# Kernel optimization log

Hardware: AMD Instinct MI355X
Metric: run time of the kernel (lower is better)

## Reference

```python
import jax, jax.numpy as jnp
from jax import lax
import numpy as np

B, N, C = 16, 8192, 256


def farthest_point_sample(pts, npoint):
    # pts: [B, N, 3]. Standard PointNet++ FPS; is_center=True -> start from the
    # point farthest from the centroid (argmax of dist-to-mean).
    b, n, _ = pts.shape
    centroid = pts.mean(axis=1, keepdims=True)                  # [B,1,3]
    d0 = jnp.sum((pts - centroid) ** 2, axis=-1)                # [B,N]
    farthest = jnp.argmax(d0, axis=-1)                          # [B]
    dist = jnp.full((b, n), 1e10, dtype=pts.dtype)

    def step(carry, _):
        dist, far = carry
        cur = jnp.take_along_axis(pts, far[:, None, None], axis=1)  # [B,1,3]
        d = jnp.sum((pts - cur) ** 2, axis=-1)                      # [B,N]
        dist = jnp.minimum(dist, d)
        new_far = jnp.argmax(dist, axis=-1)
        return (dist, new_far), far

    (_, _), idxs = lax.scan(step, (dist, farthest), None, length=npoint)
    return idxs.T  # [B, npoint]


def index_points(x, idx):
    # x: [B, N, D], idx: [B, M] -> [B, M, D]
    return jnp.take_along_axis(x, idx[:, :, None], axis=1)


def setup_inputs() -> dict:
    key = jax.random.key(0)
    k1, k2 = jax.random.split(key)
    points = jax.random.normal(k1, (B, 3, N), dtype=jnp.float32)
    features = jax.random.normal(k2, (B, C, N), dtype=jnp.float32)
    return {"points": points, "features": features, "num_points": 2048}


def reference(points, features, num_points):
    pts = jnp.swapaxes(points, -1, -2)     # [B,N,3]
    feats = jnp.swapaxes(features, -1, -2) # [B,N,C]
    idx = farthest_point_sample(pts, num_points)  # [B,M] int
    sampled_points = index_points(pts, idx)       # [B,M,3]
    sampled_features = index_points(feats, idx)   # [B,M,C]
    return sampled_points, sampled_features
```

## Files before the change

### kernel.cpp

```cpp
#include <hip/hip_runtime.h>
#include <cfloat>

#define BB 16
#define NN 8192
#define CC 256
#define NT 512
#define PPT 16
#define NPAIR (PPT / 2)
#define NWAVES (NT / 64)
#define TBLOCKS 240
#define NTILES (BB * (CC / 64) * (NN / 64))

typedef float    v2f __attribute__((ext_vector_type(2)));
typedef unsigned v2u __attribute__((ext_vector_type(2)));
typedef unsigned uu;
typedef unsigned long long ull;

#define LDS_BARRIER() __asm__ __volatile__("s_waitcnt lgkmcnt(0)\n\ts_barrier" ::: "memory")

struct SmemFPS {
  float px[NN], py[NN], pz[NN];
  ull   key[2][NWAVES];
  float red[NWAVES][3];
  float ctr[3];
};
struct SmemT {
  float tile[64][65];
};
union Smem { SmemFPS f; SmemT t; };

__device__ __forceinline__ v2f pk_sub(v2f a, v2f b) {
  v2f d;
  asm("v_pk_add_f32 %0, %1, %2 neg_lo:[0,1] neg_hi:[0,1]"
      : "=v"(d) : "v"(a), "v"(b));
  return d;
}
__device__ __forceinline__ v2f pk_mul(v2f a, v2f b) {
  v2f d;
  asm("v_pk_mul_f32 %0, %1, %2" : "=v"(d) : "v"(a), "v"(b));
  return d;
}
__device__ __forceinline__ v2f pk_add(v2f a, v2f b) {
  v2f d;
  asm("v_pk_add_f32 %0, %1, %2" : "=v"(d) : "v"(a), "v"(b));
  return d;
}

__device__ __forceinline__ uu umin2(uu a, uu b) { return a < b ? a : b; }
__device__ __forceinline__ uu umax2(uu a, uu b) { return a > b ? a : b; }

__device__ __forceinline__ ull max64(ull a, ull b) { return a > b ? a : b; }

template <int CTRL>
__device__ __forceinline__ ull dpp_max64(ull x) {
  int lo = (int)(uu)x;
  int hi = (int)(uu)(x >> 32);
  int plo = __builtin_amdgcn_update_dpp(0, lo, CTRL, 0xF, 0xF, true);
  int phi = __builtin_amdgcn_update_dpp(0, hi, CTRL, 0xF, 0xF, true);
  ull p = ((ull)(uu)phi << 32) | (uu)plo;
  return max64(x, p);
}

__device__ __forceinline__ ull wave_max63(ull k) {
  k = dpp_max64<0xB1>(k);
  k = dpp_max64<0x4E>(k);
  k = dpp_max64<0x124>(k);
  k = dpp_max64<0x128>(k);
  k = dpp_max64<0x142>(k);
  k = dpp_max64<0x143>(k);
  return k;
}

__global__ __launch_bounds__(NT)
void fps_fused_kernel(const float* __restrict__ pts,
                      const float* __restrict__ feats,
                      float* __restrict__ out_pts,
                      int* __restrict__ idx_out,
                      float* __restrict__ trans, int M, int do_trans) {
  __shared__ Smem sm;
  const int t = threadIdx.x;

  if (blockIdx.x >= BB) {
    if (!do_trans) return;
    for (int tileId = blockIdx.x - BB; tileId < NTILES; tileId += TBLOCKS) {
      int b  = tileId / ((CC / 64) * (NN / 64));
      int r  = tileId % ((CC / 64) * (NN / 64));
      int ct = r / (NN / 64);
      int nt = r % (NN / 64);
      const float* src = feats + ((size_t)b * CC + ct * 64) * NN + nt * 64;
      float* dst = trans + ((size_t)b * NN + nt * 64) * CC + ct * 64;
#pragma unroll
      for (int i = 0; i < 2; ++i) {
        int f = t + i * NT;
        int c = f >> 4, n4 = f & 15;
        float4 v = *(const float4*)(src + (size_t)c * NN + n4 * 4);
        sm.t.tile[c][n4 * 4 + 0] = v.x;
        sm.t.tile[c][n4 * 4 + 1] = v.y;
        sm.t.tile[c][n4 * 4 + 2] = v.z;
        sm.t.tile[c][n4 * 4 + 3] = v.w;
      }
      __syncthreads();
#pragma unroll
      for (int i = 0; i < 2; ++i) {
        int f = t + i * NT;
        int n = f >> 4, c4 = f & 15;
        float4 o;
        o.x = sm.t.tile[c4 * 4 + 0][n];
        o.y = sm.t.tile[c4 * 4 + 1][n];
        o.z = sm.t.tile[c4 * 4 + 2][n];
        o.w = sm.t.tile[c4 * 4 + 3][n];
        *(float4*)(dst + (size_t)n * CC + c4 * 4) = o;
      }
      __syncthreads();
    }
    return;
  }

  const int b = blockIdx.x;
  const int wave = t >> 6;
  const int lane = t & 63;
  const float* base = pts + (size_t)b * 3 * NN;

  v2f px2[NPAIR], py2[NPAIR], pz2[NPAIR];
  v2u dist2[NPAIR];
  const uu INIT = __float_as_uint(1e10f);
#pragma unroll
  for (int j = 0; j < NPAIR; ++j) {
    int n0 = t + (2 * j) * NT;
    int n1 = t + (2 * j + 1) * NT;
    float x0 = base[n0], y0 = base[NN + n0], z0 = base[2 * NN + n0];
    float x1 = base[n1], y1 = base[NN + n1], z1 = base[2 * NN + n1];
    px2[j] = (v2f){x0, x1};
    py2[j] = (v2f){y0, y1};
    pz2[j] = (v2f){z0, z1};
    sm.f.px[n0] = x0; sm.f.py[n0] = y0; sm.f.pz[n0] = z0;
    sm.f.px[n1] = x1; sm.f.py[n1] = y1; sm.f.pz[n1] = z1;
    dist2[j] = (v2u){INIT, INIT};
  }

  float sx = 0.f, sy = 0.f, sz = 0.f;
#pragma unroll
  for (int j = 0; j < NPAIR; ++j) {
    sx += px2[j].x; sx += px2[j].y;
    sy += py2[j].x; sy += py2[j].y;
    sz += pz2[j].x; sz += pz2[j].y;
  }
#pragma unroll
  for (int off = 32; off > 0; off >>= 1) {
    sx += __shfl_xor(sx, off);
    sy += __shfl_xor(sy, off);
    sz += __shfl_xor(sz, off);
  }
  if (lane == 0) { sm.f.red[wave][0] = sx; sm.f.red[wave][1] = sy; sm.f.red[wave][2] = sz; }
  __syncthreads();
  if (t == 0) {
    float gx = 0.f, gy = 0.f, gz = 0.f;
    for (int w = 0; w < NWAVES; ++w) { gx += sm.f.red[w][0]; gy += sm.f.red[w][1]; gz += sm.f.red[w][2]; }
    sm.f.ctr[0] = gx / NN; sm.f.ctr[1] = gy / NN; sm.f.ctr[2] = gz / NN;
  }
  __syncthreads();
  const float ctx = sm.f.ctr[0], cty = sm.f.ctr[1], ctz = sm.f.ctr[2];

  int ep = 0;
  int ci;

  auto reduce_tail = [&](uu v, int bk) {
    ull key = ((ull)v << 32) | (uu)(~(t + (bk << 9)));
    key = wave_max63(key);
    ep ^= 1;
    if (lane == 63) sm.f.key[ep][wave] = key;
    LDS_BARRIER();
    ull kk = sm.f.key[ep][lane & 7];
    kk = dpp_max64<0xB1>(kk);
    kk = dpp_max64<0x4E>(kk);
    kk = dpp_max64<0x124>(kk);
    ci = (int)~(uu)kk;
  };

  {
    v2f c2x = {ctx, ctx}, c2y = {cty, cty}, c2z = {ctz, ctz};
    v2u nd2[NPAIR];
    uu v = 0u;
#pragma unroll
    for (int j = 0; j < NPAIR; ++j) {
      v2f dx = pk_sub(px2[j], c2x);
      v2f dy = pk_sub(py2[j], c2y);
      v2f dz = pk_sub(pz2[j], c2z);
      v2f d = pk_add(pk_add(pk_mul(dx, dx), pk_mul(dy, dy)), pk_mul(dz, dz));
      v2u du = (v2u){__float_as_uint(d.x), __float_as_uint(d.y)};
      nd2[j] = du;
      v = umax2(v, umax2(du.x, du.y));
    }
    int bk = 0;
#pragma unroll
    for (int k = PPT - 1; k >= 0; --k) {
      uu ndk = (k & 1) ? nd2[k >> 1].y : nd2[k >> 1].x;
      if (ndk == v) bk = k;
    }
    reduce_tail(v, bk);
  }

  for (int m = 0; m < M; ++m) {
    float cx = sm.f.px[ci], cy = sm.f.py[ci], cz = sm.f.pz[ci];
    if (t == 0) {
      idx_out[b * M + m] = ci;
      size_t o = ((size_t)b * M + m) * 3;
      out_pts[o] = cx; out_pts[o + 1] = cy; out_pts[o + 2] = cz;
    }
    if (m == M - 1) break;

    v2f c2x = {cx, cx}, c2y = {cy, cy}, c2z = {cz, cz};
    v2u nd2[NPAIR];
    uu v = 0u;
#pragma unroll
    for (int j = 0; j < NPAIR; ++j) {
      v2f dx = pk_sub(px2[j], c2x);
      v2f dy = pk_sub(py2[j], c2y);
      v2f dz = pk_sub(pz2[j], c2z);
      v2f d = pk_add(pk_add(pk_mul(dx, dx), pk_mul(dy, dy)), pk_mul(dz, dz));
      v2u nd;
      nd.x = umin2(dist2[j].x, __float_as_uint(d.x));
      nd.y = umin2(dist2[j].y, __float_as_uint(d.y));
      dist2[j] = nd;
      nd2[j] = nd;
      v = umax2(v, umax2(nd.x, nd.y));
    }
    int bk = 0;
#pragma unroll
    for (int k = PPT - 1; k >= 0; --k) {
      uu ndk = (k & 1) ? nd2[k >> 1].y : nd2[k >> 1].x;
      if (ndk == v) bk = k;
    }
    reduce_tail(v, bk);
  }
}

__global__ __launch_bounds__(256)
void gather_t_kernel(const float* __restrict__ trans,
                     const int* __restrict__ idx,
                     float* __restrict__ out_f, int M) {
  int gm = blockIdx.x * 4 + (threadIdx.x >> 6);
  if (gm >= BB * M) return;
  int lane = threadIdx.x & 63;
  int b = gm / M;
  int n = idx[gm];
  float4 v = *(const float4*)(trans + ((size_t)b * NN + n) * CC + lane * 4);
  *(float4*)(out_f + (size_t)gm * CC + lane * 4) = v;
}

__global__ __launch_bounds__(CC)
void gather_kernel(const float* __restrict__ feats, const int* __restrict__ idx,
                   float* __restrict__ out_f, int M) {
  const int bm = blockIdx.x;
  const int b = bm / M;
  const int n = idx[bm];
  const int c = threadIdx.x;
  out_f[(size_t)bm * CC + c] = feats[((size_t)b * CC + c) * NN + n];
}

extern "C" void kernel_launch(void* const* d_in, const int* in_sizes, int n_in,
                              void* d_out, int out_size, void* d_ws, size_t ws_size,
                              hipStream_t stream) {
  const float* points = (const float*)d_in[0];
  const float* feats  = (const float*)d_in[1];
  int M = out_size / (BB * (3 + CC));
  if (M <= 0) M = 1;

  float* out_pts = (float*)d_out;
  float* out_f   = (float*)d_out + (size_t)BB * M * 3;

  int* idx_ws = (int*)d_ws;
  size_t idx_bytes = (((size_t)BB * M * sizeof(int)) + 255) & ~(size_t)255;
  size_t trans_bytes = (size_t)BB * NN * CC * sizeof(float);
  bool use_t = (ws_size >= idx_bytes + trans_bytes);
  float* trans = (float*)((char*)d_ws + idx_bytes);

  int grid = use_t ? (BB + TBLOCKS) : BB;
  fps_fused_kernel<<<dim3(grid), dim3(NT), 0, stream>>>(
      points, feats, out_pts, idx_ws, trans, M, use_t ? 1 : 0);

  if (use_t) {
    gather_t_kernel<<<dim3((BB * M + 3) / 4), dim3(256), 0, stream>>>(
        trans, idx_ws, out_f, M);
  } else {
    gather_kernel<<<dim3(BB * M), dim3(CC), 0, stream>>>(feats, idx_ws, out_f, M);
  }
}
```

Baseline: 1.909 ms.

## Morton-sort points per block and prune FPS distance updates with bounding spheres

Points are bucketed into a 12-bit Morton order with an LDS histogram, prefix scan and scatter, so each thread owns a spatially compact group of 16 points. Each thread keeps a bounding sphere around its group. When a wave's spheres are all farther from the new center than the cached max distance, the distance update is skipped and the cached max and index are reused. Ties break on the original index packed into the key, so the selection order is preserved. This trades a costly setup sort and extra LDS use for skipping per-iteration arithmetic, and the skip only happens when every lane in a wave prunes.

```diff
diff --git a/kernel.cpp b/kernel.cpp
--- a/kernel.cpp
+++ b/kernel.cpp
@@ -10,6 +10,7 @@
 #define NWAVES (NT / 64)
 #define TBLOCKS 240
 #define NTILES (BB * (CC / 64) * (NN / 64))
+#define NBUCK 4096
 
 typedef float    v2f __attribute__((ext_vector_type(2)));
 typedef unsigned v2u __attribute__((ext_vector_type(2)));
@@ -20,13 +21,14 @@
 
 struct SmemFPS {
   float px[NN], py[NN], pz[NN];
+  unsigned short pn[NN];
+  int   hist[NBUCK];
   ull   key[2][NWAVES];
-  float red[NWAVES][3];
-  float ctr[3];
+  float red[NWAVES][9];
+  float st9[9];
+  int   wsum[NWAVES];
 };
-struct SmemT {
-  float tile[64][65];
-};
+struct SmemT { float tile[64][65]; };
 union Smem { SmemFPS f; SmemT t; };
 
 __device__ __forceinline__ v2f pk_sub(v2f a, v2f b) {
@@ -48,7 +50,6 @@
 
 __device__ __forceinline__ uu umin2(uu a, uu b) { return a < b ? a : b; }
 __device__ __forceinline__ uu umax2(uu a, uu b) { return a > b ? a : b; }
-
 __device__ __forceinline__ ull max64(ull a, ull b) { return a > b ? a : b; }
 
 template <int CTRL>
@@ -69,6 +70,17 @@
   k = dpp_max64<0x142>(k);
   k = dpp_max64<0x143>(k);
   return k;
+}
+
+__device__ __forceinline__ int morton12(int x, int y, int z) {
+  int c = 0;
+#pragma unroll
+  for (int i = 0; i < 4; ++i) {
+    c |= ((x >> i) & 1) << (3 * i);
+    c |= ((y >> i) & 1) << (3 * i + 1);
+    c |= ((z >> i) & 1) << (3 * i + 2);
+  }
+  return c;
 }
 
 __global__ __launch_bounds__(NT)
@@ -121,51 +133,134 @@
   const int lane = t & 63;
   const float* base = pts + (size_t)b * 3 * NN;
 
+  float rx[PPT], ry[PPT], rz[PPT];
+#pragma unroll
+  for (int k = 0; k < PPT; ++k) {
+    int n = t + k * NT;
+    rx[k] = base[n]; ry[k] = base[NN + n]; rz[k] = base[2 * NN + n];
+  }
+  float sx = 0.f, sy = 0.f, sz = 0.f;
+  float mnx = rx[0], mny = ry[0], mnz = rz[0];
+  float mxx = rx[0], mxy = ry[0], mxz = rz[0];
+#pragma unroll
+  for (int k = 0; k < PPT; ++k) {
+    sx += rx[k]; sy += ry[k]; sz += rz[k];
+    mnx = fminf(mnx, rx[k]); mny = fminf(mny, ry[k]); mnz = fminf(mnz, rz[k]);
+    mxx = fmaxf(mxx, rx[k]); mxy = fmaxf(mxy, ry[k]); mxz = fmaxf(mxz, rz[k]);
+  }
+#pragma unroll
+  for (int off = 32; off > 0; off >>= 1) {
+    sx += __shfl_xor(sx, off); sy += __shfl_xor(sy, off); sz += __shfl_xor(sz, off);
+    mnx = fminf(mnx, __shfl_xor(mnx, off));
+    mny = fminf(mny, __shfl_xor(mny, off));
+    mnz = fminf(mnz, __shfl_xor(mnz, off));
+    mxx = fmaxf(mxx, __shfl_xor(mxx, off));
+    mxy = fmaxf(mxy, __shfl_xor(mxy, off));
+    mxz = fmaxf(mxz, __shfl_xor(mxz, off));
+  }
+  if (lane == 0) {
+    sm.f.red[wave][0] = sx;  sm.f.red[wave][1] = sy;  sm.f.red[wave][2] = sz;
+    sm.f.red[wave][3] = mnx; sm.f.red[wave][4] = mny; sm.f.red[wave][5] = mnz;
+    sm.f.red[wave][6] = mxx; sm.f.red[wave][7] = mxy; sm.f.red[wave][8] = mxz;
+  }
+  for (int i = t; i < NBUCK; i += NT) sm.f.hist[i] = 0;
+  __syncthreads();
+  if (t == 0) {
+    float gx = 0.f, gy = 0.f, gz = 0.f;
+    float a3 = sm.f.red[0][3], a4 = sm.f.red[0][4], a5 = sm.f.red[0][5];
+    float a6 = sm.f.red[0][6], a7 = sm.f.red[0][7], a8 = sm.f.red[0][8];
+    for (int w = 0; w < NWAVES; ++w) {
+      gx += sm.f.red[w][0]; gy += sm.f.red[w][1]; gz += sm.f.red[w][2];
+      a3 = fminf(a3, sm.f.red[w][3]); a4 = fminf(a4, sm.f.red[w][4]);
+      a5 = fminf(a5, sm.f.red[w][5]);
+      a6 = fmaxf(a6, sm.f.red[w][6]); a7 = fmaxf(a7, sm.f.red[w][7]);
+      a8 = fmaxf(a8, sm.f.red[w][8]);
+    }
+    sm.f.st9[0] = gx / NN; sm.f.st9[1] = gy / NN; sm.f.st9[2] = gz / NN;
+    sm.f.st9[3] = a3; sm.f.st9[4] = a4; sm.f.st9[5] = a5;
+    sm.f.st9[6] = a6; sm.f.st9[7] = a7; sm.f.st9[8] = a8;
+  }
+  __syncthreads();
+  const float ctx = sm.f.st9[0], cty = sm.f.st9[1], ctz = sm.f.st9[2];
+  const float qmnx = sm.f.st9[3], qmny = sm.f.st9[4], qmnz = sm.f.st9[5];
+  const float eps = 1e-30f;
+  const float sclx = 15.9999f / fmaxf(sm.f.st9[6] - qmnx, eps);
+  const float scly = 15.9999f / fmaxf(sm.f.st9[7] - qmny, eps);
+  const float sclz = 15.9999f / fmaxf(sm.f.st9[8] - qmnz, eps);
+
+  int code[PPT];
+#pragma unroll
+  for (int k = 0; k < PPT; ++k) {
+    int qx = (int)((rx[k] - qmnx) * sclx); qx = qx > 15 ? 15 : qx;
+    int qy = (int)((ry[k] - qmny) * scly); qy = qy > 15 ? 15 : qy;
+    int qz = (int)((rz[k] - qmnz) * sclz); qz = qz > 15 ? 15 : qz;
+    code[k] = morton12(qx, qy, qz);
+    atomicAdd(&sm.f.hist[code[k]], 1);
+  }
+  __syncthreads();
+
+  int loc[8]; int ssum = 0;
+#pragma unroll
+  for (int i = 0; i < 8; ++i) { loc[i] = ssum; ssum += sm.f.hist[t * 8 + i]; }
+  int sc = ssum;
+#pragma unroll
+  for (int off = 1; off < 64; off <<= 1) {
+    int o = __shfl_up(sc, off);
+    if (lane >= off) sc += o;
+  }
+  if (lane == 63) sm.f.wsum[wave] = sc;
+  __syncthreads();
+  int woff = 0;
+  for (int w = 0; w < wave; ++w) woff += sm.f.wsum[w];
+  int tbase = woff + sc - ssum;
+#pragma unroll
+  for (int i = 0; i < 8; ++i) sm.f.hist[t * 8 + i] = tbase + loc[i];
+  __syncthreads();
+
+#pragma unroll
+  for (int k = 0; k < PPT; ++k) {
+    int pos = atomicAdd(&sm.f.hist[code[k]], 1);
+    sm.f.px[pos] = rx[k]; sm.f.py[pos] = ry[k]; sm.f.pz[pos] = rz[k];
+    sm.f.pn[pos] = (unsigned short)(t + k * NT);
+  }
+  __syncthreads();
+
+  const int p0 = t * PPT;
   v2f px2[NPAIR], py2[NPAIR], pz2[NPAIR];
   v2u dist2[NPAIR];
+  uu  low[PPT];
+  float csx = 0.f, csy = 0.f, csz = 0.f;
+#pragma unroll
+  for (int k = 0; k < PPT; ++k) {
+    float x = sm.f.px[p0 + k], y = sm.f.py[p0 + k], z = sm.f.pz[p0 + k];
+    int n = (int)sm.f.pn[p0 + k];
+    if (k & 1) { px2[k >> 1].y = x; py2[k >> 1].y = y; pz2[k >> 1].y = z; }
+    else       { px2[k >> 1].x = x; py2[k >> 1].x = y * 0.f + x;
+                 px2[k >> 1].x = x; py2[k >> 1].x = y; pz2[k >> 1].x = z; }
+    low[k] = ~(uu)(((uu)n << 13) | (uu)(p0 + k));
+    csx += x; csy += y; csz += z;
+  }
+  const float ictrx = csx * 0.0625f, ictry = csy * 0.0625f, ictrz = csz * 0.0625f;
+  float r2m = 0.f;
+#pragma unroll
+  for (int k = 0; k < PPT; ++k) {
+    float x = (k & 1) ? px2[k >> 1].y : px2[k >> 1].x;
+    float y = (k & 1) ? py2[k >> 1].y : py2[k >> 1].x;
+    float z = (k & 1) ? pz2[k >> 1].y : pz2[k >> 1].x;
+    float ddx = x - ictrx, ddy = y - ictry, ddz = z - ictrz;
+    r2m = fmaxf(r2m, fmaf(ddx, ddx, fmaf(ddy, ddy, ddz * ddz)));
+  }
+  const float rr = __fsqrt_rn(r2m) * 1.0001f + 1e-7f;
   const uu INIT = __float_as_uint(1e10f);
 #pragma unroll
-  for (int j = 0; j < NPAIR; ++j) {
-    int n0 = t + (2 * j) * NT;
-    int n1 = t + (2 * j + 1) * NT;
-    float x0 = base[n0], y0 = base[NN + n0], z0 = base[2 * NN + n0];
-    float x1 = base[n1], y1 = base[NN + n1], z1 = base[2 * NN + n1];
-    px2[j] = (v2f){x0, x1};
-    py2[j] = (v2f){y0, y1};
-    pz2[j] = (v2f){z0, z1};
-    sm.f.px[n0] = x0; sm.f.py[n0] = y0; sm.f.pz[n0] = z0;
-    sm.f.px[n1] = x1; sm.f.py[n1] = y1; sm.f.pz[n1] = z1;
-    dist2[j] = (v2u){INIT, INIT};
-  }
-
-  float sx = 0.f, sy = 0.f, sz = 0.f;
-#pragma unroll
-  for (int j = 0; j < NPAIR; ++j) {
-    sx += px2[j].x; sx += px2[j].y;
-    sy += py2[j].x; sy += py2[j].y;
-    sz += pz2[j].x; sz += pz2[j].y;
-  }
-#pragma unroll
-  for (int off = 32; off > 0; off >>= 1) {
-    sx += __shfl_xor(sx, off);
-    sy += __shfl_xor(sy, off);
-    sz += __shfl_xor(sz, off);
-  }
-  if (lane == 0) { sm.f.red[wave][0] = sx; sm.f.red[wave][1] = sy; sm.f.red[wave][2] = sz; }
-  __syncthreads();
-  if (t == 0) {
-    float gx = 0.f, gy = 0.f, gz = 0.f;
-    for (int w = 0; w < NWAVES; ++w) { gx += sm.f.red[w][0]; gy += sm.f.red[w][1]; gz += sm.f.red[w][2]; }
-    sm.f.ctr[0] = gx / NN; sm.f.ctr[1] = gy / NN; sm.f.ctr[2] = gz / NN;
-  }
-  __syncthreads();
-  const float ctx = sm.f.ctr[0], cty = sm.f.ctr[1], ctz = sm.f.ctr[2];
-
-  int ep = 0;
-  int ci;
-
-  auto reduce_tail = [&](uu v, int bk) {
-    ull key = ((ull)v << 32) | (uu)(~(t + (bk << 9)));
+  for (int j = 0; j < NPAIR; ++j) dist2[j] = (v2u){INIT, INIT};
+  uu vcache = 0x7f800000u;
+  uu lowcache = 0u;
+
+  int ep = 0, cpos = 0, corig = 0;
+
+  auto reduce_tail = [&](uu v, uu blow) {
+    ull key = ((ull)v << 32) | blow;
     key = wave_max63(key);
     ep ^= 1;
     if (lane == 63) sm.f.key[ep][wave] = key;
@@ -174,7 +269,9 @@
     kk = dpp_max64<0xB1>(kk);
     kk = dpp_max64<0x4E>(kk);
     kk = dpp_max64<0x124>(kk);
-    ci = (int)~(uu)kk;
+    uu X = ~(uu)kk;
+    cpos = (int)(X & 0x1FFFu);
+    corig = (int)(X >> 13);
   };
 
   {
@@ -191,47 +288,62 @@
       nd2[j] = du;
       v = umax2(v, umax2(du.x, du.y));
     }
-    int bk = 0;
-#pragma unroll
-    for (int k = PPT - 1; k >= 0; --k) {
+    uu blow = 0u;
+#pragma unroll
+    for (int k = 0; k < PPT; ++k) {
       uu ndk = (k & 1) ? nd2[k >> 1].y : nd2[k >> 1].x;
-      if (ndk == v) bk = k;
-    }
-    reduce_tail(v, bk);
+      uu tmp = umax2(blow, low[k]);
+      blow = (ndk == v) ? tmp : blow;
+    }
+    reduce_tail(v, blow);
   }
 
   for (int m = 0; m < M; ++m) {
-    float cx = sm.f.px[ci], cy = sm.f.py[ci], cz = sm.f.pz[ci];
+    float cx = sm.f.px[cpos], cy = sm.f.py[cpos], cz = sm.f.pz[cpos];
     if (t == 0) {
-      idx_out[b * M + m] = ci;
+      idx_out[b * M + m] = corig;
       size_t o = ((size_t)b * M + m) * 3;
       out_pts[o] = cx; out_pts[o + 1] = cy; out_pts[o + 2] = cz;
     }
     if (m == M - 1) break;
 
-    v2f c2x = {cx, cx}, c2y = {cy, cy}, c2z = {cz, cz};
-    v2u nd2[NPAIR];
-    uu v = 0u;
-#pragma unroll
-    for (int j = 0; j < NPAIR; ++j) {
-      v2f dx = pk_sub(px2[j], c2x);
-      v2f dy = pk_sub(py2[j], c2y);
-      v2f dz = pk_sub(pz2[j], c2z);
-      v2f d = pk_add(pk_add(pk_mul(dx, dx), pk_mul(dy, dy)), pk_mul(dz, dz));
-      v2u nd;
-      nd.x = umin2(dist2[j].x, __float_as_uint(d.x));
-      nd.y = umin2(dist2[j].y, __float_as_uint(d.y));
-      dist2[j] = nd;
-      nd2[j] = nd;
-      v = umax2(v, umax2(nd.x, nd.y));
-    }
-    int bk = 0;
-#pragma unroll
-    for (int k = PPT - 1; k >= 0; --k) {
-      uu ndk = (k & 1) ? nd2[k >> 1].y : nd2[k >> 1].x;
-      if (ndk == v) bk = k;
-    }
-    reduce_tail(v, bk);
+    float dxc = cx - ictrx, dyc = cy - ictry, dzc = cz - ictrz;
+    float dc2 = fmaf(dxc, dxc, fmaf(dyc, dyc, dzc * dzc));
+    float dcf = __fsqrt_rn(dc2);
+    float lbf = dcf * 0.9999f - rr;
+    float lb2 = lbf * lbf * 0.9999f;
+    bool prune = (lbf > 0.f) && (__float_as_uint(lb2) > vcache);
+
+    uu v, blow;
+    if (__all(prune)) {
+      v = vcache; blow = lowcache;
+    } else {
+      v2f c2x = {cx, cx}, c2y = {cy, cy}, c2z = {cz, cz};
+      v2u nd2[NPAIR];
+      v = 0u;
+#pragma unroll
+      for (int j = 0; j < NPAIR; ++j) {
+        v2f dx = pk_sub(px2[j], c2x);
+        v2f dy = pk_sub(py2[j], c2y);
+        v2f dz = pk_sub(pz2[j], c2z);
+        v2f d = pk_add(pk_add(pk_mul(dx, dx), pk_mul(dy, dy)), pk_mul(dz, dz));
+        v2u nd;
+        nd.x = umin2(dist2[j].x, __float_as_uint(d.x));
+        nd.y = umin2(dist2[j].y, __float_as_uint(d.y));
+        dist2[j] = nd;
+        nd2[j] = nd;
+        v = umax2(v, umax2(nd.x, nd.y));
+      }
+      blow = 0u;
+#pragma unroll
+      for (int k = 0; k < PPT; ++k) {
+        uu ndk = (k & 1) ? nd2[k >> 1].y : nd2[k >> 1].x;
+        uu tmp = umax2(blow, low[k]);
+        blow = (ndk == v) ? tmp : blow;
+      }
+      vcache = v; lowcache = blow;
+    }
+    reduce_tail(v, blow);
   }
 }
 
```

Measured after the change: 2.136 ms. 1.12x slower.
